# Optimization experiments

Measured on AMD Instinct MI355X. Metric: run time of the kernel, lower is better.

## Reference

```python
import jax, jax.numpy as jnp
import numpy as np

B, T, C, H = 2, 2048, 1024, 16
HD = C // H  # head dim = 64


def setup_inputs() -> dict:
    key = jax.random.key(0)
    ks = jax.random.split(key, 5)
    s = 1.0 / np.sqrt(C)
    return {
        "x": jax.random.normal(ks[0], (B, T, C), dtype=jnp.float32),
        "W_attn": jax.random.normal(ks[1], (3 * C, C), dtype=jnp.float32) * s,
        "b_attn": jax.random.normal(ks[2], (3 * C,), dtype=jnp.float32) * 0.02,
        "W_proj": jax.random.normal(ks[3], (C, C), dtype=jnp.float32) * s,
        "b_proj": jax.random.normal(ks[4], (C,), dtype=jnp.float32) * 0.02,
    }


def reference(x, W_attn, b_attn, W_proj, b_proj):
    Bx, Tx, Cx = x.shape
    # fused QKV projection (torch Linear: x @ W.T + b)
    qkv = x @ W_attn.T + b_attn                      # [B,T,3C]
    q, k, v = jnp.split(qkv, 3, axis=-1)
    # [B,T,C] -> [B,H,T,hd]
    q = q.reshape(Bx, Tx, H, HD).transpose(0, 2, 1, 3)
    k = k.reshape(Bx, Tx, H, HD).transpose(0, 2, 1, 3)
    v = v.reshape(Bx, Tx, H, HD).transpose(0, 2, 1, 3)
    scale = 1.0 / np.sqrt(HD)
    att = jnp.einsum('bhqd,bhkd->bhqk', q, k) * scale  # [B,H,T,T]
    causal = jnp.tril(jnp.ones((Tx, Tx), dtype=bool))
    att = jnp.where(causal[None, None], att, -jnp.inf)
    att = jax.nn.softmax(att, axis=-1)
    y = jnp.einsum('bhqk,bhkd->bhqd', att, v)          # [B,H,T,hd]
    y = y.transpose(0, 2, 1, 3).reshape(Bx, Tx, Cx)
    return y @ W_proj.T + b_proj
```

## Files before the change

### kernel.cpp

```cpp
#include <hip/hip_runtime.h>

typedef unsigned short ushort_t;
typedef __bf16 bf16x8 __attribute__((ext_vector_type(8)));
typedef float f32x4 __attribute__((ext_vector_type(4)));
typedef unsigned u32x4 __attribute__((ext_vector_type(4)));

__device__ inline ushort_t f2bf(float f) {
  unsigned int u = __builtin_bit_cast(unsigned int, f);
  u += 0x7fff + ((u >> 16) & 1);
  return (ushort_t)(u >> 16);
}

__device__ inline unsigned pk_bf(float a, float b) {
  unsigned r;
  asm("v_cvt_pk_bf16_f32 %0, %1, %2" : "=v"(r) : "v"(a), "v"(b));
  return r;
}

__device__ inline void async_ld16(const ushort_t* g, const ushort_t* l) {
  __builtin_amdgcn_global_load_lds(
      (const __attribute__((address_space(1))) void*)g,
      (__attribute__((address_space(3))) void*)l, 16, 0, 0);
}

template <int IMM>
__device__ inline void waitcnt_barrier() {
  asm volatile("" ::: "memory");
  __builtin_amdgcn_s_waitcnt(IMM);
  __builtin_amdgcn_s_barrier();
  asm volatile("" ::: "memory");
}

__global__ void cvt_all(const float* __restrict__ x, const float* __restrict__ wa,
                        const float* __restrict__ wp, ushort_t* __restrict__ xb,
                        ushort_t* __restrict__ wab, ushort_t* __restrict__ wpb) {
  int i = blockIdx.x * 256 + threadIdx.x;
  const float* src;
  ushort_t* dst;
  int off;
  if (i < 1048576) { src = x; dst = xb; off = i; }
  else if (i < 1835008) { src = wa; dst = wab; off = i - 1048576; }
  else { src = wp; dst = wpb; off = i - 1835008; }
  float4 f = ((const float4*)src)[off];
  unsigned long long p = (unsigned long long)f2bf(f.x)
      | ((unsigned long long)f2bf(f.y) << 16)
      | ((unsigned long long)f2bf(f.z) << 32)
      | ((unsigned long long)f2bf(f.w) << 48);
  ((unsigned long long*)dst)[off] = p;
}

template <int BM, int BN, int IM, int JN, int MODE, int TPB>
__global__ __launch_bounds__(TPB) void gemm_bt(
    const ushort_t* __restrict__ A, const ushort_t* __restrict__ B,
    const float* __restrict__ bias, float* __restrict__ Cf,
    ushort_t* __restrict__ Cb, ushort_t* __restrict__ vtb,
    int M, int N, int K, int ldc, float qscale) {
  constexpr int NWN = BN / (JN * 16);
  constexpr int NL = (BM + BN) * 32 / (TPB * 8);
  constexpr int WIMM = 0x0F70 | NL;
  __shared__ __align__(16) ushort_t As[3][BM * 32];
  __shared__ __align__(16) ushort_t Bs[3][BN * 32];
  const int tid = threadIdx.x;
  const int wave = tid >> 6, lane = tid & 63;
  const int quad = lane >> 4, l16 = lane & 15;
  const int wr = wave / NWN, wc = wave % NWN;
  const int wm = wr * IM * 16, wn = wc * JN * 16;
  const int m0 = blockIdx.y * BM, n0 = blockIdx.x * BN;
  const ushort_t* Ag = A + (size_t)m0 * K;
  const ushort_t* Bg = B + (size_t)n0 * K;
  const int slot = (quad ^ ((l16 >> 1) & 3)) * 8;
  f32x4 acc[IM][JN] = {};

  auto stage = [&](int kt, int bsel) {
    int k0 = kt * 32;
#pragma unroll
    for (int p = 0; p < BM * 4 / TPB; ++p) {
      int ci = p * TPB + tid;
      int row = ci >> 2, ch = (ci & 3) ^ ((ci >> 3) & 3);
      async_ld16(Ag + (size_t)row * K + k0 + ch * 8, As[bsel] + (p * TPB + wave * 64) * 8);
    }
#pragma unroll
    for (int p = 0; p < BN * 4 / TPB; ++p) {
      int ci = p * TPB + tid;
      int row = ci >> 2, ch = (ci & 3) ^ ((ci >> 3) & 3);
      async_ld16(Bg + (size_t)row * K + k0 + ch * 8, Bs[bsel] + (p * TPB + wave * 64) * 8);
    }
  };

  const int KT = K / 32;
  stage(0, 0);
  stage(1, 1);
  for (int kt = 0; kt < KT; ++kt) {
    waitcnt_barrier<WIMM>();
    if (kt + 2 < KT) stage(kt + 2, (kt + 2) % 3);
    const ushort_t* Ac = As[kt % 3];
    const ushort_t* Bc = Bs[kt % 3];
    bf16x8 af[IM], bfr[JN];
#pragma unroll
    for (int i = 0; i < IM; ++i)
      af[i] = *(const bf16x8*)(Ac + (wm + i * 16 + l16) * 32 + slot);
#pragma unroll
    for (int j = 0; j < JN; ++j)
      bfr[j] = *(const bf16x8*)(Bc + (wn + j * 16 + l16) * 32 + slot);
#pragma unroll
    for (int i = 0; i < IM; ++i)
#pragma unroll
      for (int j = 0; j < JN; ++j)
        acc[i][j] = __builtin_amdgcn_mfma_f32_16x16x32_bf16(af[i], bfr[j], acc[i][j], 0, 0, 0);
  }

  if (MODE == 1 && n0 >= 2048) {
#pragma unroll
    for (int j = 0; j < JN; ++j) {
      int col = n0 + wn + j * 16 + l16;
      int cv = col - 2048;
      float bv = bias[col];
      size_t rowbase = ((size_t)(cv >> 6)) * 64 + (cv & 63);
#pragma unroll
      for (int i = 0; i < IM; ++i) {
        int rowb = m0 + wm + i * 16 + quad * 4;
        int bb = rowb >> 11, t = rowb & 2047;
        uint2 pp;
        pp.x = pk_bf(acc[i][j][0] + bv, acc[i][j][1] + bv);
        pp.y = pk_bf(acc[i][j][2] + bv, acc[i][j][3] + bv);
        *(uint2*)(vtb + (((size_t)bb * 1024 + rowbase) * 2048 + t)) = pp;
      }
    }
    return;
  }
#pragma unroll
  for (int j = 0; j < JN; ++j) {
    int col = n0 + wn + j * 16 + l16;
    float bv = bias[col];
    float sc = (MODE == 1 && col < 1024) ? qscale : 1.0f;
#pragma unroll
    for (int i = 0; i < IM; ++i)
#pragma unroll
      for (int r = 0; r < 4; ++r) {
        int row = m0 + wm + i * 16 + quad * 4 + r;
        float v = (acc[i][j][r] + bv) * sc;
        if (MODE == 1)
          Cb[(size_t)row * ldc + col] = f2bf(v);
        else
          Cf[(size_t)row * ldc + col] = v;
      }
  }
}

__global__ __launch_bounds__(512, 2) void flash12(
    const ushort_t* __restrict__ qk, const ushort_t* __restrict__ vt,
    ushort_t* __restrict__ y, float* __restrict__ pO, float* __restrict__ pl) {
  __shared__ __align__(16) ushort_t Kb[2][2][4096];
  __shared__ __align__(16) ushort_t Vb[2][2][4096];
  const int tid = threadIdx.x, wave = tid >> 6, lane = tid & 63;
  const int quad = lane >> 4, l16 = lane & 15;
  const int r7 = l16 & 7;
  const int fK = (l16 & 3) | (((l16 >> 2) & 1) << 2);
  const int kbase = (16 * (l16 >> 2) + (l16 & 3)) * 64;
  const int w = blockIdx.x, bh = blockIdx.y;
  const int b = bh >> 4, h = bh & 15;
  const int bT = b * 2048;
  const int nseg = (w & 1) ? 2 : 1;
  u32x4 onesw;
  onesw[0] = 0x3F803F80u; onesw[1] = 0x3F803F80u;
  onesw[2] = 0x3F803F80u; onesw[3] = 0x3F803F80u;
  const bf16x8 ones = __builtin_bit_cast(bf16x8, onesw);

  auto stage1 = [&](int t, int bsel, int u) {
    int k0 = t * 64;
    int row = tid >> 3;
    int chk = (tid & 7) ^ ((row & 3) | (((row >> 4) & 1) << 2));
    int chv = (tid & 7) ^ (row & 7);
    async_ld16(qk + (size_t)(bT + k0 + row) * 2048 + 1024 + h * 64 + chk * 8,
               Kb[bsel][u] + wave * 512);
    async_ld16(vt + (size_t)(bh * 64 + row) * 2048 + k0 + chv * 8,
               Vb[bsel][u] + wave * 512);
  };

  for (int seg = 0; seg < nseg; ++seg) {
    int j, tbeg, tend, isfin;
    if (w & 1) {
      if (seg == 0) { j = 15 - (w >> 1); tbeg = 17; tend = 2 * j + 2; isfin = 0; }
      else          { j = w >> 1;        tbeg = 0;  tend = 2 * j + 2; isfin = 1; }
    } else          { j = 15 - (w >> 1); tbeg = 0;  tend = 17;        isfin = 0; }
    const int qt0 = j * 128;
    const int qw = qt0 + wave * 16;
    const int qloc = qw + l16;

    bf16x8 qf[2];
    {
      const ushort_t* qrow = qk + (size_t)(bT + qloc) * 2048 + h * 64 + quad * 8;
      qf[0] = *(const bf16x8*)(qrow);
      qf[1] = *(const bf16x8*)(qrow + 32);
    }

    auto stageS = [&](int s, int bsel) {
      int t0 = tbeg + 2 * s;
      stage1(t0, bsel, 0);
      if (t0 + 1 < tend) stage1(t0 + 1, bsel, 1);
    };

    f32x4 o[4] = {};
    f32x4 lacc = {};
    const int NSs = (tend - tbeg + 1) >> 1;

    if (seg) __syncthreads();
    stageS(0, 0);
    for (int s = 0; s < NSs; ++s) {
      const int cur = s & 1;
      waitcnt_barrier<0x0F70>();
      if (s + 1 < NSs) stageS(s + 1, cur ^ 1);
      __builtin_amdgcn_s_setprio(1);
      const int t0 = tbeg + 2 * s;
#pragma unroll
      for (int u = 0; u < 2; ++u) {
        if (u == 1 && t0 + 1 >= tend) break;
        const int kt = t0 + u;
        const ushort_t* Kc = Kb[cur][u];
        const ushort_t* Vc = Vb[cur][u];
        bf16x8 kf[4][2];
#pragma unroll
        for (int jj = 0; jj < 4; ++jj)
#pragma unroll
          for (int ks = 0; ks < 2; ++ks)
            kf[jj][ks] = *(const bf16x8*)(Kc + kbase + jj * 256 + (((ks * 4 + quad) ^ fK) * 8));
        f32x4 sr[4] = {};
#pragma unroll
        for (int ks = 0; ks < 2; ++ks)
#pragma unroll
          for (int jj = 0; jj < 4; ++jj)
            sr[jj] = __builtin_amdgcn_mfma_f32_16x16x32_bf16(kf[jj][ks], qf[ks], sr[jj], 0, 0, 0);
        if (kt >= 2 * j) {
#pragma unroll
          for (int jj = 0; jj < 4; ++jj)
#pragma unroll
            for (int r = 0; r < 4; ++r)
              if (kt * 64 + quad * 16 + jj * 4 + r > qloc) sr[jj][r] = -1e30f;
        }
#pragma unroll
        for (int jj = 0; jj < 4; ++jj)
#pragma unroll
          for (int r = 0; r < 4; ++r)
            sr[jj][r] = exp2f(sr[jj][r]);
        bf16x8 pf[2];
#pragma unroll
        for (int ks = 0; ks < 2; ++ks) {
          u32x4 wd;
          wd[0] = pk_bf(sr[2 * ks][0], sr[2 * ks][1]);
          wd[1] = pk_bf(sr[2 * ks][2], sr[2 * ks][3]);
          wd[2] = pk_bf(sr[2 * ks + 1][0], sr[2 * ks + 1][1]);
          wd[3] = pk_bf(sr[2 * ks + 1][2], sr[2 * ks + 1][3]);
          pf[ks] = __builtin_bit_cast(bf16x8, wd);
        }
        lacc = __builtin_amdgcn_mfma_f32_16x16x32_bf16(ones, pf[0], lacc, 0, 0, 0);
        lacc = __builtin_amdgcn_mfma_f32_16x16x32_bf16(ones, pf[1], lacc, 0, 0, 0);
#pragma unroll
        for (int ks = 0; ks < 2; ++ks)
#pragma unroll
          for (int jj = 0; jj < 4; ++jj) {
            bf16x8 vf = *(const bf16x8*)(Vc + (jj * 16 + l16) * 64 + (((ks + 2 * quad) ^ r7) * 8));
            o[jj] = __builtin_amdgcn_mfma_f32_16x16x32_bf16(vf, pf[ks], o[jj], 0, 0, 0);
          }
      }
      __builtin_amdgcn_s_setprio(0);
    }

    float l = lacc[0];
    const int rowloc = wave * 16 + l16;

    if (isfin) {
      float inv = 1.f / l;
      size_t row = (size_t)(bT + qt0 + rowloc);
#pragma unroll
      for (int jj = 0; jj < 4; ++jj) {
        uint2 pp;
        pp.x = pk_bf(o[jj][0] * inv, o[jj][1] * inv);
        pp.y = pk_bf(o[jj][2] * inv, o[jj][3] * inv);
        *(uint2*)(y + row * 1024 + h * 64 + jj * 16 + quad * 4) = pp;
      }
    } else {
      const int tile = bh * 8 + (j - 8);
      const int slot = w & 1;
      float* po = pO + ((size_t)(tile * 2 + slot)) * 8192;
#pragma unroll
      for (int jj = 0; jj < 4; ++jj)
        *(f32x4*)(po + rowloc * 64 + jj * 16 + quad * 4) = o[jj];
      if (quad == 0) pl[(tile * 2 + slot) * 128 + rowloc] = l;
    }
  }
}

__global__ __launch_bounds__(256) void combine(
    const float* __restrict__ pO, const float* __restrict__ pl,
    ushort_t* __restrict__ y) {
  const int tile = blockIdx.x;
  const int bh = tile >> 3, j = (tile & 7) + 8;
  const int b = bh >> 4, h = bh & 15;
  const int row = threadIdx.x >> 1;
  const int c0 = (threadIdx.x & 1) * 32;
  const float* p0 = pO + (size_t)(tile * 2 + 0) * 8192 + row * 64 + c0;
  const float* p1 = pO + (size_t)(tile * 2 + 1) * 8192 + row * 64 + c0;
  const float inv = 1.f / (pl[(tile * 2) * 128 + row] + pl[(tile * 2 + 1) * 128 + row]);
  ushort_t* yr = y + (size_t)(b * 2048 + j * 128 + row) * 1024 + h * 64 + c0;
#pragma unroll
  for (int c = 0; c < 8; ++c) {
    f32x4 a = *(const f32x4*)(p0 + c * 4);
    f32x4 bb = *(const f32x4*)(p1 + c * 4);
    uint2 pp;
    pp.x = pk_bf((a[0] + bb[0]) * inv, (a[1] + bb[1]) * inv);
    pp.y = pk_bf((a[2] + bb[2]) * inv, (a[3] + bb[3]) * inv);
    *(uint2*)(yr + c * 4) = pp;
  }
}

extern "C" void kernel_launch(void* const* d_in, const int* in_sizes, int n_in,
                              void* d_out, int out_size, void* d_ws, size_t ws_size,
                              hipStream_t stream) {
  const float* x  = (const float*)d_in[0];
  const float* Wa = (const float*)d_in[1];
  const float* ba = (const float*)d_in[2];
  const float* Wp = (const float*)d_in[3];
  const float* bp = (const float*)d_in[4];
  float* out = (float*)d_out;
  char* ws = (char*)d_ws;
  ushort_t* xb  = (ushort_t*)(ws);
  ushort_t* Wab = (ushort_t*)(ws + 8388608);
  ushort_t* Wpb = (ushort_t*)(ws + 14680064);
  ushort_t* qkb = (ushort_t*)(ws + 16777216);
  ushort_t* yb  = (ushort_t*)(ws + 33554432);
  ushort_t* vtb = (ushort_t*)(ws + 41943040);
  float*    pO  = (float*)(ws + 67108864);
  float*    pl  = (float*)(ws + 83886080);

  cvt_all<<<8192, 256, 0, stream>>>(x, Wa, Wp, xb, Wab, Wpb);
  gemm_bt<128, 128, 4, 2, 1, 512><<<dim3(24, 32), 512, 0, stream>>>(
      xb, Wab, ba, nullptr, qkb, vtb, 4096, 3072, 1024, 2048, 0.18033688011112042f);
  flash12<<<dim3(16, 32), 512, 0, stream>>>(qkb, vtb, yb, pO, pl);
  combine<<<256, 256, 0, stream>>>(pO, pl, yb);
  gemm_bt<128, 128, 4, 2, 0, 512><<<dim3(8, 32), 512, 0, stream>>>(
      yb, Wpb, bp, out, nullptr, nullptr, 4096, 1024, 1024, 1024, 1.0f);
}
```

Baseline: 179.2 us.

## Load K/V fragments directly from global memory instead of staging through LDS

The flash attention kernel drops the double-buffered async global-to-LDS staging of K and V tiles and the per-step barriers. Each wave now reads its K and V MFMA fragments straight from global memory (relying on L2/L1 reuse across the eight waves), and launch bounds rise to allow 4 blocks per CU since no LDS is used. This removes LDS traffic and synchronisation but makes each wave issue redundant, less coalesced global loads with no explicit prefetch, so latency hiding depends on occupancy.

```diff
diff --git a/kernel.cpp b/kernel.cpp
--- a/kernel.cpp
+++ b/kernel.cpp
@@ -147,35 +147,23 @@
   }
 }
 
-__global__ __launch_bounds__(512, 2) void flash12(
+__global__ __launch_bounds__(512, 4) void flash14(
     const ushort_t* __restrict__ qk, const ushort_t* __restrict__ vt,
     ushort_t* __restrict__ y, float* __restrict__ pO, float* __restrict__ pl) {
-  __shared__ __align__(16) ushort_t Kb[2][2][4096];
-  __shared__ __align__(16) ushort_t Vb[2][2][4096];
   const int tid = threadIdx.x, wave = tid >> 6, lane = tid & 63;
   const int quad = lane >> 4, l16 = lane & 15;
-  const int r7 = l16 & 7;
-  const int fK = (l16 & 3) | (((l16 >> 2) & 1) << 2);
-  const int kbase = (16 * (l16 >> 2) + (l16 & 3)) * 64;
   const int w = blockIdx.x, bh = blockIdx.y;
   const int b = bh >> 4, h = bh & 15;
   const int bT = b * 2048;
   const int nseg = (w & 1) ? 2 : 1;
+  const int krow0 = 16 * (l16 >> 2) + (l16 & 3);
   u32x4 onesw;
   onesw[0] = 0x3F803F80u; onesw[1] = 0x3F803F80u;
   onesw[2] = 0x3F803F80u; onesw[3] = 0x3F803F80u;
   const bf16x8 ones = __builtin_bit_cast(bf16x8, onesw);
 
-  auto stage1 = [&](int t, int bsel, int u) {
-    int k0 = t * 64;
-    int row = tid >> 3;
-    int chk = (tid & 7) ^ ((row & 3) | (((row >> 4) & 1) << 2));
-    int chv = (tid & 7) ^ (row & 7);
-    async_ld16(qk + (size_t)(bT + k0 + row) * 2048 + 1024 + h * 64 + chk * 8,
-               Kb[bsel][u] + wave * 512);
-    async_ld16(vt + (size_t)(bh * 64 + row) * 2048 + k0 + chv * 8,
-               Vb[bsel][u] + wave * 512);
-  };
+  const ushort_t* Kl = qk + (size_t)(bT + krow0) * 2048 + 1024 + h * 64 + quad * 8;
+  const ushort_t* Vl = vt + (size_t)(bh * 64 + l16) * 2048 + quad * 16;
 
   for (int seg = 0; seg < nseg; ++seg) {
     int j, tbeg, tend, isfin;
@@ -194,75 +182,59 @@
       qf[1] = *(const bf16x8*)(qrow + 32);
     }
 
-    auto stageS = [&](int s, int bsel) {
-      int t0 = tbeg + 2 * s;
-      stage1(t0, bsel, 0);
-      if (t0 + 1 < tend) stage1(t0 + 1, bsel, 1);
-    };
-
     f32x4 o[4] = {};
     f32x4 lacc = {};
-    const int NSs = (tend - tbeg + 1) >> 1;
-
-    if (seg) __syncthreads();
-    stageS(0, 0);
-    for (int s = 0; s < NSs; ++s) {
-      const int cur = s & 1;
-      waitcnt_barrier<0x0F70>();
-      if (s + 1 < NSs) stageS(s + 1, cur ^ 1);
-      __builtin_amdgcn_s_setprio(1);
-      const int t0 = tbeg + 2 * s;
-#pragma unroll
-      for (int u = 0; u < 2; ++u) {
-        if (u == 1 && t0 + 1 >= tend) break;
-        const int kt = t0 + u;
-        const ushort_t* Kc = Kb[cur][u];
-        const ushort_t* Vc = Vb[cur][u];
-        bf16x8 kf[4][2];
+
+    for (int t = tbeg; t < tend; ++t) {
+      const ushort_t* Kt = Kl + (size_t)t * 131072;
+      const ushort_t* Vt = Vl + t * 64;
+      bf16x8 kf[4][2];
+#pragma unroll
+      for (int jj = 0; jj < 4; ++jj)
+#pragma unroll
+        for (int ks = 0; ks < 2; ++ks)
+          kf[jj][ks] = *(const bf16x8*)(Kt + (size_t)jj * 8192 + ks * 32);
+      f32x4 sr[4] = {};
+#pragma unroll
+      for (int ks = 0; ks < 2; ++ks)
 #pragma unroll
         for (int jj = 0; jj < 4; ++jj)
-#pragma unroll
-          for (int ks = 0; ks < 2; ++ks)
-            kf[jj][ks] = *(const bf16x8*)(Kc + kbase + jj * 256 + (((ks * 4 + quad) ^ fK) * 8));
-        f32x4 sr[4] = {};
+          sr[jj] = __builtin_amdgcn_mfma_f32_16x16x32_bf16(kf[jj][ks], qf[ks], sr[jj], 0, 0, 0);
+      bf16x8 vf[4][2];
+#pragma unroll
+      for (int jj = 0; jj < 4; ++jj)
 #pragma unroll
         for (int ks = 0; ks < 2; ++ks)
-#pragma unroll
-          for (int jj = 0; jj < 4; ++jj)
-            sr[jj] = __builtin_amdgcn_mfma_f32_16x16x32_bf16(kf[jj][ks], qf[ks], sr[jj], 0, 0, 0);
-        if (kt >= 2 * j) {
-#pragma unroll
-          for (int jj = 0; jj < 4; ++jj)
-#pragma unroll
-            for (int r = 0; r < 4; ++r)
-              if (kt * 64 + quad * 16 + jj * 4 + r > qloc) sr[jj][r] = -1e30f;
-        }
+          vf[jj][ks] = *(const bf16x8*)(Vt + (size_t)jj * 32768 + ks * 8);
+      if (t >= 2 * j) {
 #pragma unroll
         for (int jj = 0; jj < 4; ++jj)
 #pragma unroll
           for (int r = 0; r < 4; ++r)
-            sr[jj][r] = exp2f(sr[jj][r]);
-        bf16x8 pf[2];
-#pragma unroll
-        for (int ks = 0; ks < 2; ++ks) {
-          u32x4 wd;
-          wd[0] = pk_bf(sr[2 * ks][0], sr[2 * ks][1]);
-          wd[1] = pk_bf(sr[2 * ks][2], sr[2 * ks][3]);
-          wd[2] = pk_bf(sr[2 * ks + 1][0], sr[2 * ks + 1][1]);
-          wd[3] = pk_bf(sr[2 * ks + 1][2], sr[2 * ks + 1][3]);
-          pf[ks] = __builtin_bit_cast(bf16x8, wd);
-        }
-        lacc = __builtin_amdgcn_mfma_f32_16x16x32_bf16(ones, pf[0], lacc, 0, 0, 0);
-        lacc = __builtin_amdgcn_mfma_f32_16x16x32_bf16(ones, pf[1], lacc, 0, 0, 0);
-#pragma unroll
-        for (int ks = 0; ks < 2; ++ks)
-#pragma unroll
-          for (int jj = 0; jj < 4; ++jj) {
-            bf16x8 vf = *(const bf16x8*)(Vc + (jj * 16 + l16) * 64 + (((ks + 2 * quad) ^ r7) * 8));
-            o[jj] = __builtin_amdgcn_mfma_f32_16x16x32_bf16(vf, pf[ks], o[jj], 0, 0, 0);
-          }
-      }
-      __builtin_amdgcn_s_setprio(0);
+            if (t * 64 + quad * 16 + jj * 4 + r > qloc) sr[jj][r] = -1e30f;
+      }
+#pragma unroll
+      for (int jj = 0; jj < 4; ++jj)
+#pragma unroll
+        for (int r = 0; r < 4; ++r)
+          sr[jj][r] = exp2f(sr[jj][r]);
+      bf16x8 pf[2];
+#pragma unroll
+      for (int ks = 0; ks < 2; ++ks) {
+        u32x4 wd;
+        wd[0] = pk_bf(sr[2 * ks][0], sr[2 * ks][1]);
+        wd[1] = pk_bf(sr[2 * ks][2], sr[2 * ks][3]);
+        wd[2] = pk_bf(sr[2 * ks + 1][0], sr[2 * ks + 1][1]);
+        wd[3] = pk_bf(sr[2 * ks + 1][2], sr[2 * ks + 1][3]);
+        pf[ks] = __builtin_bit_cast(bf16x8, wd);
+      }
+      lacc = __builtin_amdgcn_mfma_f32_16x16x32_bf16(ones, pf[0], lacc, 0, 0, 0);
+      lacc = __builtin_amdgcn_mfma_f32_16x16x32_bf16(ones, pf[1], lacc, 0, 0, 0);
+#pragma unroll
+      for (int ks = 0; ks < 2; ++ks)
+#pragma unroll
+        for (int jj = 0; jj < 4; ++jj)
+          o[jj] = __builtin_amdgcn_mfma_f32_16x16x32_bf16(vf[jj][ks], pf[ks], o[jj], 0, 0, 0);
     }
 
     float l = lacc[0];
@@ -335,7 +307,7 @@
   cvt_all<<<8192, 256, 0, stream>>>(x, Wa, Wp, xb, Wab, Wpb);
   gemm_bt<128, 128, 4, 2, 1, 512><<<dim3(24, 32), 512, 0, stream>>>(
       xb, Wab, ba, nullptr, qkb, vtb, 4096, 3072, 1024, 2048, 0.18033688011112042f);
-  flash12<<<dim3(16, 32), 512, 0, stream>>>(qkb, vtb, yb, pO, pl);
+  flash14<<<dim3(16, 32), 512, 0, stream>>>(qkb, vtb, yb, pO, pl);
   combine<<<256, 256, 0, stream>>>(pO, pl, yb);
   gemm_bt<128, 128, 4, 2, 0, 512><<<dim3(8, 32), 512, 0, stream>>>(
       yb, Wpb, bp, out, nullptr, nullptr, 4096, 1024, 1024, 1024, 1.0f);
```

Result: slower. 270.4 us (+50.9%).
